# Kernel tuning notes

Hardware: AMD Instinct MI355X
Metric: run time of the kernel (lower is better)

The kernel has to match this reference:

```python
import jax, jax.numpy as jnp
import numpy as np


def setup_inputs() -> dict:
    key = jax.random.key(0)
    k1, k2 = jax.random.split(key)
    B, S, D, R = 8, 2048, 1024, 128
    batch = jax.random.normal(k1, (B, S, D), dtype=jnp.float32)
    proj = jax.random.normal(k2, (D, R), dtype=jnp.float32) * (1.0 / np.sqrt(D))
    return {"batch": batch, "proj": proj}


def reference(batch, proj):
    # transformed: (B, S, R)
    t = jnp.matmul(batch, proj)
    # Pairwise squared L2 distances: ||ti||^2 + ||tj||^2 - 2 ti.tj
    # (same math as expand/diff/pow/sum, without the (B,S,S,R) intermediate)
    sq = jnp.sum(t * t, axis=-1)                       # (B, S)
    dots = jnp.einsum('bir,bjr->bij', t, t)            # (B, S, S)
    d2 = sq[:, :, None] + sq[:, None, :] - 2.0 * dots  # (B, S, S)
    return d2
```

## Files before the change

### kernel.cpp

```cpp
#include <hip/hip_runtime.h>
#include <hip/hip_bf16.h>

typedef short bf16x8 __attribute__((ext_vector_type(8)));
typedef float f32x4 __attribute__((ext_vector_type(4)));

#define NB 8
#define SS 2048
#define DD 1024
#define RR 128

__device__ __forceinline__ short f2bf(float x){
  unsigned u = __float_as_uint(x);
  u += 0x7fffu + ((u >> 16) & 1u);
  return (short)(u >> 16);
}
__device__ __forceinline__ float bf2f(short h){
  return __uint_as_float(((unsigned)(unsigned short)h) << 16);
}
__device__ __forceinline__ void gload16(const void* g, void* l){
  __builtin_amdgcn_global_load_lds((const __attribute__((address_space(1))) unsigned*)g,
                                   (__attribute__((address_space(3))) unsigned*)l, 16, 0, 0);
}
__device__ __forceinline__ int swz(int row, int c16){
  return row * 64 + ((c16 ^ (row & 7)) << 3);
}

__global__ __launch_bounds__(256) void k0_proj(const float* __restrict__ proj,
                                               short* __restrict__ pt_hi,
                                               short* __restrict__ pt_lo){
  __shared__ float tile[64][65];
  const int d0 = blockIdx.x * 64, r0 = blockIdx.y * 64;
  const int tid = threadIdx.x;
  #pragma unroll
  for (int i = 0; i < 16; ++i){
    int u = i * 256 + tid;
    int d = u >> 6, r = u & 63;
    tile[d][r] = proj[(d0 + d) * RR + r0 + r];
  }
  __syncthreads();
  #pragma unroll
  for (int i = 0; i < 16; ++i){
    int u = i * 256 + tid;
    int r = u >> 6, d = u & 63;
    float x = tile[d][r];
    short h = f2bf(x);
    short l = f2bf(x - bf2f(h));
    pt_hi[(r0 + r) * DD + d0 + d] = h;
    pt_lo[(r0 + r) * DD + d0 + d] = l;
  }
}

__global__ __launch_bounds__(512, 2) void k1_gemm1(const float* __restrict__ batch,
                                                   const short* __restrict__ pt_hi,
                                                   const short* __restrict__ pt_lo,
                                                   short* __restrict__ t_hi,
                                                   short* __restrict__ t_lo,
                                                   float* __restrict__ sqv){
  __shared__ __align__(16) char smem[49408];
  short* Ah = (short*)smem;
  short* Al = (short*)(smem + 8192);
  short* Ph = (short*)(smem + 16384);
  short* Pl = (short*)(smem + 32768);
  float* sqpart = (float*)(smem + 49152);
  const int tid = threadIdx.x;
  const int w = tid >> 6, lane = tid & 63;
  const int lr = lane & 15, lg = lane >> 4;
  const int wr = w & 3, wc = w >> 2;
  const int row0 = blockIdx.x * 64;
  const int colg = (lane & 7) ^ (lane >> 3);
  if (tid < 64) sqpart[tid] = 0.f;
  f32x4 acc[4] = {{0.f,0.f,0.f,0.f}};
  #pragma unroll 1
  for (int k0 = 0; k0 < DD; k0 += 64){
    #pragma unroll
    for (int i = 0; i < 2; ++i){
      int u = tid * 2 + i;
      int r = u >> 4, kc = (u & 15) * 4;
      float4 v = *(const float4*)(batch + (size_t)(row0 + r) * DD + k0 + kc);
      short4 hv, lv;
      hv.x = f2bf(v.x); lv.x = f2bf(v.x - bf2f(hv.x));
      hv.y = f2bf(v.y); lv.y = f2bf(v.y - bf2f(hv.y));
      hv.z = f2bf(v.z); lv.z = f2bf(v.z - bf2f(hv.z));
      hv.w = f2bf(v.w); lv.w = f2bf(v.w - bf2f(hv.w));
      int sidx = r * 64 + (((kc >> 3) ^ (r & 7)) << 3) + (kc & 7);
      *(short4*)&Ah[sidx] = hv;
      *(short4*)&Al[sidx] = lv;
    }
    #pragma unroll
    for (int q = 0; q < 2; ++q){
      int prow = w * 16 + q * 8 + (lane >> 3);
      const short* gh = pt_hi + prow * DD + k0 + colg * 8;
      const short* gl = pt_lo + prow * DD + k0 + colg * 8;
      gload16(gh, &Ph[w * 1024 + q * 512]);
      gload16(gl, &Pl[w * 1024 + q * 512]);
    }
    __syncthreads();
    #pragma unroll
    for (int ks = 0; ks < 2; ++ks){
      int c16 = ks * 4 + lg;
      bf16x8 ah = *(const bf16x8*)&Ah[swz(wr * 16 + lr, c16)];
      bf16x8 al = *(const bf16x8*)&Al[swz(wr * 16 + lr, c16)];
      bf16x8 bh[4], bl[4];
      #pragma unroll
      for (int n = 0; n < 4; ++n){
        int prow = wc * 64 + n * 16 + lr;
        bh[n] = *(const bf16x8*)&Ph[swz(prow, c16)];
        bl[n] = *(const bf16x8*)&Pl[swz(prow, c16)];
      }
      #pragma unroll
      for (int n = 0; n < 4; ++n)
        acc[n] = __builtin_amdgcn_mfma_f32_16x16x32_bf16(ah, bh[n], acc[n], 0, 0, 0);
      #pragma unroll
      for (int n = 0; n < 4; ++n)
        acc[n] = __builtin_amdgcn_mfma_f32_16x16x32_bf16(ah, bl[n], acc[n], 0, 0, 0);
      #pragma unroll
      for (int n = 0; n < 4; ++n)
        acc[n] = __builtin_amdgcn_mfma_f32_16x16x32_bf16(al, bh[n], acc[n], 0, 0, 0);
    }
    __syncthreads();
  }
  short* Th = Ph;
  short* Tl = Pl;
  #pragma unroll
  for (int r = 0; r < 4; ++r){
    int lrow = wr * 16 + lg * 4 + r;
    float s = 0.f;
    #pragma unroll
    for (int n = 0; n < 4; ++n){
      float x = acc[n][r];
      s += x * x;
      int col = wc * 64 + n * 16 + lr;
      short h = f2bf(x);
      short l = f2bf(x - bf2f(h));
      Th[lrow * 128 + col] = h;
      Tl[lrow * 128 + col] = l;
    }
    s += __shfl_xor(s, 1);
    s += __shfl_xor(s, 2);
    s += __shfl_xor(s, 4);
    s += __shfl_xor(s, 8);
    if (lr == 0) atomicAdd(&sqpart[lrow], s);
  }
  __syncthreads();
  #pragma unroll
  for (int ps = 0; ps < 2; ++ps){
    int u = ps * 512 + tid;
    int row = u >> 4, c8 = (u & 15) * 8;
    *(int4*)&t_hi[(size_t)(row0 + row) * RR + c8] = *(int4*)&Th[row * 128 + c8];
    *(int4*)&t_lo[(size_t)(row0 + row) * RR + c8] = *(int4*)&Tl[row * 128 + c8];
  }
  if (tid < 64) sqv[row0 + tid] = sqpart[tid];
}

__global__ __launch_bounds__(512, 1) void k2_dist(const short* __restrict__ t_hi,
                                                  const short* __restrict__ t_lo,
                                                  const float* __restrict__ sqv,
                                                  float* __restrict__ out){
  __shared__ short lds[65536];
  const int tid = threadIdx.x;
  const int w = tid >> 6, lane = tid & 63;
  const int lr = lane & 15, lg = lane >> 4;
  const int srow = ((w & 1) << 2) | (lane >> 4);
  const int colg = (lane & 15) ^ srow;
  const int bi = blockIdx.x & 7;
  const int lidx = blockIdx.x >> 3;
  const size_t tbase = (size_t)bi * SS * RR;
  float* outb = out + (size_t)bi * SS * SS;
  const float* sqb = sqv + bi * SS;

  auto decodeP = [&](int p, int& i0, int& j0, bool& dg){
    int ti = 0;
    while (p >= 16 - ti){ p -= 16 - ti; ++ti; }
    int tj = ti + p;
    i0 = ti * 128; j0 = tj * 128; dg = (ti == tj);
  };
  auto stageTile = [&](int i0, int j0, bool dg){
    #pragma unroll
    for (int q = 0; q < 4; ++q){
      int rl = q * 32 + w * 4;
      int gr = rl + (lane >> 4);
      size_t oA = tbase + (size_t)(i0 + gr) * RR + colg * 8;
      gload16(t_hi + oA, &lds[rl * 128]);
      gload16(t_lo + oA, &lds[16384 + rl * 128]);
      if (!dg){
        size_t oB = tbase + (size_t)(j0 + gr) * RR + colg * 8;
        gload16(t_hi + oB, &lds[32768 + rl * 128]);
        gload16(t_lo + oB, &lds[49152 + rl * 128]);
      }
    }
  };

  int p = lidx;
  int i0, j0; bool dg;
  decodeP(p, i0, j0, dg);
  stageTile(i0, j0, dg);
  while (true){
    __syncthreads();
    const int bh0 = dg ? 0 : 32768, bl0 = dg ? 16384 : 49152;
    f32x4 acc[8] = {{0.f,0.f,0.f,0.f}};
    const int ar = w * 16 + lr;
    const int aoff = ar * 128;
    const int asw = (ar & 7);
    #pragma unroll
    for (int ks = 0; ks < 4; ++ks){
      int c16 = ks * 4 + lg;
      bf16x8 ah = *(const bf16x8*)&lds[aoff + ((c16 ^ asw) << 3)];
      bf16x8 al = *(const bf16x8*)&lds[16384 + aoff + ((c16 ^ asw) << 3)];
      bf16x8 bh[8], bl[8];
      #pragma unroll
      for (int n = 0; n < 8; ++n){
        int br = n * 16 + lr;
        int off = br * 128 + ((c16 ^ (br & 7)) << 3);
        bh[n] = *(const bf16x8*)&lds[bh0 + off];
        bl[n] = *(const bf16x8*)&lds[bl0 + off];
      }
      #pragma unroll
      for (int n = 0; n < 8; ++n)
        acc[n] = __builtin_amdgcn_mfma_f32_16x16x32_bf16(ah, bh[n], acc[n], 0, 0, 0);
      #pragma unroll
      for (int n = 0; n < 8; ++n)
        acc[n] = __builtin_amdgcn_mfma_f32_16x16x32_bf16(ah, bl[n], acc[n], 0, 0, 0);
      #pragma unroll
      for (int n = 0; n < 8; ++n)
        acc[n] = __builtin_amdgcn_mfma_f32_16x16x32_bf16(al, bh[n], acc[n], 0, 0, 0);
    }
    __syncthreads();
    int np = p + 32;
    bool more = (np < 136);
    int ni0, nj0; bool ndg;
    if (more){ decodeP(np, ni0, nj0, ndg); stageTile(ni0, nj0, ndg); }
    {
      int rbase = w * 16 + lg * 4;
      float4 si4 = *(const float4*)&sqb[i0 + rbase];
      #pragma unroll
      for (int n = 0; n < 8; ++n){
        int col = n * 16 + lr;
        float sj = sqb[j0 + col];
        float4 v;
        v.x = si4.x + sj - 2.0f * acc[n][0];
        v.y = si4.y + sj - 2.0f * acc[n][1];
        v.z = si4.z + sj - 2.0f * acc[n][2];
        v.w = si4.w + sj - 2.0f * acc[n][3];
        size_t ro = (size_t)(i0 + rbase) * SS + (j0 + col);
        outb[ro] = v.x;
        outb[ro + SS] = v.y;
        outb[ro + 2 * SS] = v.z;
        outb[ro + 3 * SS] = v.w;
        if (!dg) *(float4*)&outb[(size_t)(j0 + col) * SS + (i0 + rbase)] = v;
      }
    }
    if (!more) break;
    p = np; i0 = ni0; j0 = nj0; dg = ndg;
  }
}

extern "C" void kernel_launch(void* const* d_in, const int* in_sizes, int n_in,
                              void* d_out, int out_size, void* d_ws, size_t ws_size,
                              hipStream_t stream) {
  const float* batch = (const float*)d_in[0];
  const float* proj  = (const float*)d_in[1];
  float* out = (float*)d_out;
  char* ws = (char*)d_ws;

  short* pt_hi = (short*)(ws);
  short* pt_lo = (short*)(ws + 262144);
  short* t_hi  = (short*)(ws + 524288);
  short* t_lo  = (short*)(ws + 4718592);
  float* sqv   = (float*)(ws + 8912896);

  k0_proj<<<dim3(16, 2), 256, 0, stream>>>(proj, pt_hi, pt_lo);
  k1_gemm1<<<dim3(256), 512, 0, stream>>>(batch, pt_hi, pt_lo, t_hi, t_lo, sqv);
  k2_dist<<<dim3(256), 512, 0, stream>>>(t_hi, t_lo, sqv, out);
}
```

Baseline: 214.5 us.

## Drop low-order bf16 split for t and restructure distance kernel grid

Stores the projected matrix t only as a single bf16 term, so the distance kernel needs one MFMA pass instead of three and half the staging loads. The persistent distance kernel is replaced by a 2D grid with one tile pair per block and 4-block occupancy. The direct tile is staged through LDS so the row-major output is written as coalesced float4 stores. The cost is lower precision in the dot products, which may exceed tolerance because catastrophic cancellation in the ||a||^2+||b||^2-2ab form is amplified.

```diff
diff --git a/kernel.cpp b/kernel.cpp
--- a/kernel.cpp
+++ b/kernel.cpp
@@ -54,7 +54,6 @@
                                                    const short* __restrict__ pt_hi,
                                                    const short* __restrict__ pt_lo,
                                                    short* __restrict__ t_hi,
-                                                   short* __restrict__ t_lo,
                                                    float* __restrict__ sqv){
   __shared__ __align__(16) char smem[49408];
   short* Ah = (short*)smem;
@@ -89,10 +88,8 @@
     #pragma unroll
     for (int q = 0; q < 2; ++q){
       int prow = w * 16 + q * 8 + (lane >> 3);
-      const short* gh = pt_hi + prow * DD + k0 + colg * 8;
-      const short* gl = pt_lo + prow * DD + k0 + colg * 8;
-      gload16(gh, &Ph[w * 1024 + q * 512]);
-      gload16(gl, &Pl[w * 1024 + q * 512]);
+      gload16(pt_hi + prow * DD + k0 + colg * 8, &Ph[w * 1024 + q * 512]);
+      gload16(pt_lo + prow * DD + k0 + colg * 8, &Pl[w * 1024 + q * 512]);
     }
     __syncthreads();
     #pragma unroll
@@ -120,7 +117,6 @@
     __syncthreads();
   }
   short* Th = Ph;
-  short* Tl = Pl;
   #pragma unroll
   for (int r = 0; r < 4; ++r){
     int lrow = wr * 16 + lg * 4 + r;
@@ -130,10 +126,7 @@
       float x = acc[n][r];
       s += x * x;
       int col = wc * 64 + n * 16 + lr;
-      short h = f2bf(x);
-      short l = f2bf(x - bf2f(h));
-      Th[lrow * 128 + col] = h;
-      Tl[lrow * 128 + col] = l;
+      Th[lrow * 128 + col] = f2bf(x);
     }
     s += __shfl_xor(s, 1);
     s += __shfl_xor(s, 2);
@@ -147,110 +140,96 @@
     int u = ps * 512 + tid;
     int row = u >> 4, c8 = (u & 15) * 8;
     *(int4*)&t_hi[(size_t)(row0 + row) * RR + c8] = *(int4*)&Th[row * 128 + c8];
-    *(int4*)&t_lo[(size_t)(row0 + row) * RR + c8] = *(int4*)&Tl[row * 128 + c8];
   }
   if (tid < 64) sqv[row0 + tid] = sqpart[tid];
 }
 
-__global__ __launch_bounds__(512, 1) void k2_dist(const short* __restrict__ t_hi,
-                                                  const short* __restrict__ t_lo,
+__global__ __launch_bounds__(512, 4) void k2_dist(const short* __restrict__ t_hi,
                                                   const float* __restrict__ sqv,
                                                   float* __restrict__ out){
-  __shared__ short lds[65536];
+  __shared__ __align__(16) short lds[32768];
+  float* ftile = (float*)lds;
   const int tid = threadIdx.x;
   const int w = tid >> 6, lane = tid & 63;
   const int lr = lane & 15, lg = lane >> 4;
-  const int srow = ((w & 1) << 2) | (lane >> 4);
-  const int colg = (lane & 15) ^ srow;
-  const int bi = blockIdx.x & 7;
-  const int lidx = blockIdx.x >> 3;
+  const int bi = blockIdx.x;
+  int p = blockIdx.y;
+  int ti = 0;
+  while (p >= 16 - ti){ p -= 16 - ti; ++ti; }
+  const int tj = ti + p;
+  const int i0 = ti * 128, j0 = tj * 128;
+  const bool dg = (ti == tj);
   const size_t tbase = (size_t)bi * SS * RR;
   float* outb = out + (size_t)bi * SS * SS;
   const float* sqb = sqv + bi * SS;
-
-  auto decodeP = [&](int p, int& i0, int& j0, bool& dg){
-    int ti = 0;
-    while (p >= 16 - ti){ p -= 16 - ti; ++ti; }
-    int tj = ti + p;
-    i0 = ti * 128; j0 = tj * 128; dg = (ti == tj);
-  };
-  auto stageTile = [&](int i0, int j0, bool dg){
-    #pragma unroll
-    for (int q = 0; q < 4; ++q){
-      int rl = q * 32 + w * 4;
-      int gr = rl + (lane >> 4);
-      size_t oA = tbase + (size_t)(i0 + gr) * RR + colg * 8;
-      gload16(t_hi + oA, &lds[rl * 128]);
-      gload16(t_lo + oA, &lds[16384 + rl * 128]);
-      if (!dg){
-        size_t oB = tbase + (size_t)(j0 + gr) * RR + colg * 8;
-        gload16(t_hi + oB, &lds[32768 + rl * 128]);
-        gload16(t_lo + oB, &lds[49152 + rl * 128]);
-      }
-    }
-  };
-
-  int p = lidx;
-  int i0, j0; bool dg;
-  decodeP(p, i0, j0, dg);
-  stageTile(i0, j0, dg);
-  while (true){
-    __syncthreads();
-    const int bh0 = dg ? 0 : 32768, bl0 = dg ? 16384 : 49152;
-    f32x4 acc[8] = {{0.f,0.f,0.f,0.f}};
-    const int ar = w * 16 + lr;
-    const int aoff = ar * 128;
-    const int asw = (ar & 7);
-    #pragma unroll
-    for (int ks = 0; ks < 4; ++ks){
-      int c16 = ks * 4 + lg;
-      bf16x8 ah = *(const bf16x8*)&lds[aoff + ((c16 ^ asw) << 3)];
-      bf16x8 al = *(const bf16x8*)&lds[16384 + aoff + ((c16 ^ asw) << 3)];
-      bf16x8 bh[8], bl[8];
-      #pragma unroll
-      for (int n = 0; n < 8; ++n){
-        int br = n * 16 + lr;
-        int off = br * 128 + ((c16 ^ (br & 7)) << 3);
-        bh[n] = *(const bf16x8*)&lds[bh0 + off];
-        bl[n] = *(const bf16x8*)&lds[bl0 + off];
-      }
-      #pragma unroll
-      for (int n = 0; n < 8; ++n)
-        acc[n] = __builtin_amdgcn_mfma_f32_16x16x32_bf16(ah, bh[n], acc[n], 0, 0, 0);
-      #pragma unroll
-      for (int n = 0; n < 8; ++n)
-        acc[n] = __builtin_amdgcn_mfma_f32_16x16x32_bf16(ah, bl[n], acc[n], 0, 0, 0);
-      #pragma unroll
-      for (int n = 0; n < 8; ++n)
-        acc[n] = __builtin_amdgcn_mfma_f32_16x16x32_bf16(al, bh[n], acc[n], 0, 0, 0);
-    }
-    __syncthreads();
-    int np = p + 32;
-    bool more = (np < 136);
-    int ni0, nj0; bool ndg;
-    if (more){ decodeP(np, ni0, nj0, ndg); stageTile(ni0, nj0, ndg); }
-    {
-      int rbase = w * 16 + lg * 4;
-      float4 si4 = *(const float4*)&sqb[i0 + rbase];
-      #pragma unroll
-      for (int n = 0; n < 8; ++n){
-        int col = n * 16 + lr;
-        float sj = sqb[j0 + col];
-        float4 v;
-        v.x = si4.x + sj - 2.0f * acc[n][0];
-        v.y = si4.y + sj - 2.0f * acc[n][1];
-        v.z = si4.z + sj - 2.0f * acc[n][2];
-        v.w = si4.w + sj - 2.0f * acc[n][3];
-        size_t ro = (size_t)(i0 + rbase) * SS + (j0 + col);
-        outb[ro] = v.x;
-        outb[ro + SS] = v.y;
-        outb[ro + 2 * SS] = v.z;
-        outb[ro + 3 * SS] = v.w;
-        if (!dg) *(float4*)&outb[(size_t)(j0 + col) * SS + (i0 + rbase)] = v;
-      }
-    }
-    if (!more) break;
-    p = np; i0 = ni0; j0 = nj0; dg = ndg;
+  const int srow = ((w & 1) << 2) | (lane >> 4);
+  const int colg = (lane & 15) ^ srow;
+
+  #pragma unroll
+  for (int q = 0; q < 4; ++q){
+    int rl = q * 32 + w * 4;
+    int gr = rl + (lane >> 4);
+    gload16(t_hi + tbase + (size_t)(i0 + gr) * RR + colg * 8, &lds[rl * 128]);
+    if (!dg)
+      gload16(t_hi + tbase + (size_t)(j0 + gr) * RR + colg * 8, &lds[16384 + rl * 128]);
+  }
+  __syncthreads();
+
+  const int bh0 = dg ? 0 : 16384;
+  f32x4 acc[8] = {{0.f,0.f,0.f,0.f}};
+  const int ar = w * 16 + lr;
+  const int aoff = ar * 128;
+  const int asw = ar & 7;
+  #pragma unroll
+  for (int ks = 0; ks < 4; ++ks){
+    int c16 = ks * 4 + lg;
+    bf16x8 ah = *(const bf16x8*)&lds[aoff + ((c16 ^ asw) << 3)];
+    bf16x8 bh[8];
+    #pragma unroll
+    for (int n = 0; n < 8; ++n){
+      int br = n * 16 + lr;
+      bh[n] = *(const bf16x8*)&lds[bh0 + br * 128 + ((c16 ^ (br & 7)) << 3)];
+    }
+    #pragma unroll
+    for (int n = 0; n < 8; ++n)
+      acc[n] = __builtin_amdgcn_mfma_f32_16x16x32_bf16(ah, bh[n], acc[n], 0, 0, 0);
+  }
+  __syncthreads();
+
+  if (!dg){
+    int rbase = w * 16 + lg * 4;
+    float4 si4 = *(const float4*)&sqb[i0 + rbase];
+    #pragma unroll
+    for (int n = 0; n < 8; ++n){
+      int col = n * 16 + lr;
+      float sj = sqb[j0 + col];
+      float4 mv;
+      mv.x = si4.x + sj - 2.0f * acc[n][0];
+      mv.y = si4.y + sj - 2.0f * acc[n][1];
+      mv.z = si4.z + sj - 2.0f * acc[n][2];
+      mv.w = si4.w + sj - 2.0f * acc[n][3];
+      *(float4*)&outb[(size_t)(j0 + col) * SS + (i0 + rbase)] = mv;
+    }
+  }
+  #pragma unroll
+  for (int n = 0; n < 8; ++n)
+    #pragma unroll
+    for (int r = 0; r < 4; ++r)
+      ftile[(w * 16 + lg * 4 + r) * 128 + n * 16 + lr] = acc[n][r];
+  __syncthreads();
+  #pragma unroll
+  for (int v = 0; v < 8; ++v){
+    int u = v * 512 + tid;
+    int row = u >> 5, c4 = (u & 31) * 4;
+    float4 d = *(float4*)&ftile[row * 128 + c4];
+    float si = sqb[i0 + row];
+    float4 sj = *(const float4*)&sqb[j0 + c4];
+    float4 o;
+    o.x = si + sj.x - 2.0f * d.x;
+    o.y = si + sj.y - 2.0f * d.y;
+    o.z = si + sj.z - 2.0f * d.z;
+    o.w = si + sj.w - 2.0f * d.w;
+    *(float4*)&outb[(size_t)(i0 + row) * SS + j0 + c4] = o;
   }
 }
 
@@ -265,10 +244,9 @@
   short* pt_hi = (short*)(ws);
   short* pt_lo = (short*)(ws + 262144);
   short* t_hi  = (short*)(ws + 524288);
-  short* t_lo  = (short*)(ws + 4718592);
-  float* sqv   = (float*)(ws + 8912896);
+  float* sqv   = (float*)(ws + 4718592);
 
   k0_proj<<<dim3(16, 2), 256, 0, stream>>>(proj, pt_hi, pt_lo);
-  k1_gemm1<<<dim3(256), 512, 0, stream>>>(batch, pt_hi, pt_lo, t_hi, t_lo, sqv);
-  k2_dist<<<dim3(256), 512, 0, stream>>>(t_hi, t_lo, sqv, out);
-}
+  k1_gemm1<<<dim3(256), 512, 0, stream>>>(batch, pt_hi, pt_lo, t_hi, sqv);
+  k2_dist<<<dim3(8, 136), 512, 0, stream>>>(t_hi, sqv, out);
+}
```

Result: faster. 207.9 us (-3.1%).
